# Performance work log

Hardware: AMD Instinct MI355X
Metric: run time of the kernel (lower is better)

## Reference

```python
import jax, jax.numpy as jnp
import numpy as np

TOP_K = 8  # num_experts_per_tok


def setup_inputs() -> dict:
    key = jax.random.key(0)
    k1, k2, k3 = jax.random.split(key, 3)
    B, S, H, E = 4, 4096, 2048, 64
    hidden_states = jax.random.normal(k1, (B, S, H), dtype=jnp.float32)
    router_weight = jax.random.normal(k2, (E, H), dtype=jnp.float32)
    router_bias = jnp.zeros((E,), dtype=jnp.float32)
    expert_bias = jax.random.normal(k3, (E, H), dtype=jnp.float32) * 0.1
    return {
        "hidden_states": hidden_states,
        "router_weight": router_weight,
        "router_bias": router_bias,
        "expert_bias": expert_bias,
    }


def reference(hidden_states, router_weight, router_bias, expert_bias):
    B, S, H = hidden_states.shape
    flat = hidden_states.reshape(B * S, H)  # [T, H]
    # Router: linear -> softmax -> top-k
    logits = jnp.einsum("th,eh->te", flat, router_weight) + router_bias
    scores = jax.nn.softmax(logits, axis=-1)
    topk_w, topk_idx = jax.lax.top_k(scores, TOP_K)  # [T, K]
    # Dispatch/combine collapses to: combined[t,k] = x[t] + expert_bias[idx[t,k]]
    # output[t] = sum_k w[t,k] * combined[t,k]
    #          = x[t] * sum_k w[t,k] + sum_k w[t,k] * expert_bias[idx[t,k]]
    gathered_bias = expert_bias[topk_idx]  # [T, K, H]
    out = flat * jnp.sum(topk_w, axis=-1, keepdims=True) + jnp.einsum(
        "tk,tkh->th", topk_w, gathered_bias
    )
    return out.reshape(B, S, H)
```

## Files before the change

kernel.cpp:

```cpp
#include <hip/hip_runtime.h>
#include <hip/hip_bf16.h>
#include <float.h>

#define H 2048
#define E 64
#define TOPK 8
#define RT 16
#define TT 8
#define NT 512

typedef __attribute__((ext_vector_type(8))) short bf16x8;
typedef __attribute__((ext_vector_type(4))) float f32x4;
typedef __attribute__((ext_vector_type(4))) unsigned short us4;

__device__ __forceinline__ unsigned short f2bf(float f) {
  unsigned u = __float_as_uint(f);
  u += 0x7fffu + ((u >> 16) & 1u);
  return (unsigned short)(u >> 16);
}
__device__ __forceinline__ float bf2f(unsigned short s) {
  return __uint_as_float(((unsigned)s) << 16);
}
__device__ __forceinline__ float wred_max(float v) {
#pragma unroll
  for (int o = 32; o > 0; o >>= 1) v = fmaxf(v, __shfl_xor(v, o));
  return v;
}
__device__ __forceinline__ float wred_sum(float v) {
#pragma unroll
  for (int o = 32; o > 0; o >>= 1) v += __shfl_xor(v, o);
  return v;
}

__global__ __launch_bounds__(256) void cvt_kernel(const float* __restrict__ W,
                                                  const float* __restrict__ eb,
                                                  unsigned short* __restrict__ Wb,
                                                  unsigned short* __restrict__ Bb) {
  int i = (blockIdx.x * 256 + threadIdx.x) * 4;
  const float* src;
  unsigned short* dst;
  int off;
  if (i < E * H) { src = W; dst = Wb; off = i; }
  else           { src = eb; dst = Bb; off = i - E * H; }
  float4 v = *(const float4*)(src + off);
  us4 r;
  r[0] = f2bf(v.x); r[1] = f2bf(v.y); r[2] = f2bf(v.z); r[3] = f2bf(v.w);
  *(us4*)(dst + off) = r;
}

__global__ __launch_bounds__(256, 4) void router_kernel(
    const float* __restrict__ x, const unsigned short* __restrict__ Wb,
    const float* __restrict__ rb, float* __restrict__ msw_g,
    float* __restrict__ mw_g, int* __restrict__ mi_g) {
  __shared__ float lgs[4][RT][E + 1];
  const int tid = threadIdx.x;
  const int wv = tid >> 6, lane = tid & 63, quad = lane >> 4, m = lane & 15;
  const int t0 = (blockIdx.x * 4 + wv) * RT;

  f32x4 acc0 = {0.f,0.f,0.f,0.f}, acc1 = {0.f,0.f,0.f,0.f};
  f32x4 acc2 = {0.f,0.f,0.f,0.f}, acc3 = {0.f,0.f,0.f,0.f};
  const float* xp = x + (size_t)(t0 + m) * H + quad * 8;
  const unsigned short* wp = Wb + (size_t)m * H + quad * 8;
#pragma unroll 4
  for (int it = 0; it < H / 32; ++it) {
    float4 p = *(const float4*)(xp + it * 32);
    float4 q = *(const float4*)(xp + it * 32 + 4);
    bf16x8 av;
    av[0] = (short)f2bf(p.x); av[1] = (short)f2bf(p.y);
    av[2] = (short)f2bf(p.z); av[3] = (short)f2bf(p.w);
    av[4] = (short)f2bf(q.x); av[5] = (short)f2bf(q.y);
    av[6] = (short)f2bf(q.z); av[7] = (short)f2bf(q.w);
    bf16x8 b0 = *(const bf16x8*)(wp + (size_t)0 * 16 * H + it * 32);
    bf16x8 b1 = *(const bf16x8*)(wp + (size_t)1 * 16 * H + it * 32);
    bf16x8 b2 = *(const bf16x8*)(wp + (size_t)2 * 16 * H + it * 32);
    bf16x8 b3 = *(const bf16x8*)(wp + (size_t)3 * 16 * H + it * 32);
    acc0 = __builtin_amdgcn_mfma_f32_16x16x32_bf16(av, b0, acc0, 0, 0, 0);
    acc1 = __builtin_amdgcn_mfma_f32_16x16x32_bf16(av, b1, acc1, 0, 0, 0);
    acc2 = __builtin_amdgcn_mfma_f32_16x16x32_bf16(av, b2, acc2, 0, 0, 0);
    acc3 = __builtin_amdgcn_mfma_f32_16x16x32_bf16(av, b3, acc3, 0, 0, 0);
  }
#pragma unroll
  for (int r = 0; r < 4; ++r) {
    const int row = quad * 4 + r;
    lgs[wv][row][ 0 + m] = acc0[r];
    lgs[wv][row][16 + m] = acc1[r];
    lgs[wv][row][32 + m] = acc2[r];
    lgs[wv][row][48 + m] = acc3[r];
  }
  const float rbl = rb[lane];
  for (int t = 0; t < RT; ++t) {
    float l = lgs[wv][t][lane] + rbl;
    const float mx = wred_max(l);
    const float p = expf(l - mx);
    const float inv = 1.f / wred_sum(p);
    float sumw = 0.f, lsel = l;
    float mywk = 0.f;
    int myoff = 0;
#pragma unroll
    for (int k = 0; k < TOPK; ++k) {
      const float mk = wred_max(lsel);
      const unsigned long long b = __ballot(lsel == mk);
      const int idx = __ffsll(b) - 1;
      const float wk = expf(mk - mx) * inv;
      sumw += wk;
      if (lane == k) { mywk = wk; myoff = idx * H; }
      if (lane == idx) lsel = -FLT_MAX;
    }
    const int tt = t0 + t;
    if (lane == 0) msw_g[tt] = sumw;
    if (lane < TOPK) {
      mw_g[(size_t)tt * TOPK + lane] = mywk;
      mi_g[(size_t)tt * TOPK + lane] = myoff;
    }
  }
}

__global__ __launch_bounds__(256, 4) void combine_kernel(
    const float* __restrict__ x, const unsigned short* __restrict__ Bb,
    const float* __restrict__ msw_g, const float* __restrict__ mw_g,
    const int* __restrict__ mi_g, float* __restrict__ out) {
  const int tid = threadIdx.x;
  const int wv = tid >> 6, lane = tid & 63;
  const int t = blockIdx.x * 4 + wv;
  const float sw = msw_g[t];
  const float4 w0 = *(const float4*)(mw_g + (size_t)t * TOPK);
  const float4 w1 = *(const float4*)(mw_g + (size_t)t * TOPK + 4);
  const int4  e0 = *(const int4*)(mi_g + (size_t)t * TOPK);
  const int4  e1 = *(const int4*)(mi_g + (size_t)t * TOPK + 4);
  const float wks[8] = {w0.x, w0.y, w0.z, w0.w, w1.x, w1.y, w1.z, w1.w};
  const int   ofs[8] = {e0.x, e0.y, e0.z, e0.w, e1.x, e1.y, e1.z, e1.w};
  const float* xr = x + (size_t)t * H;
  float* orow = out + (size_t)t * H;
#pragma unroll
  for (int ch = 0; ch < 4; ++ch) {
    const int c8 = ch * 512 + lane * 8;
    const float4 xa = *(const float4*)(xr + c8);
    const float4 xb = *(const float4*)(xr + c8 + 4);
    float o[8] = {xa.x * sw, xa.y * sw, xa.z * sw, xa.w * sw,
                  xb.x * sw, xb.y * sw, xb.z * sw, xb.w * sw};
#pragma unroll
    for (int k = 0; k < TOPK; ++k) {
      const bf16x8 bv = *(const bf16x8*)(Bb + ofs[k] + c8);
      const float wk = wks[k];
#pragma unroll
      for (int i = 0; i < 8; ++i) o[i] += wk * bf2f((unsigned short)bv[i]);
    }
    *(float4*)(orow + c8)     = make_float4(o[0], o[1], o[2], o[3]);
    *(float4*)(orow + c8 + 4) = make_float4(o[4], o[5], o[6], o[7]);
  }
}

template <bool USE_WS>
__global__ __launch_bounds__(NT, 8) void moe_kernel(
    const float* __restrict__ x, const float* __restrict__ W,
    const float* __restrict__ rb, const float* __restrict__ eb,
    const unsigned short* __restrict__ Wb, const unsigned short* __restrict__ Bb,
    float* __restrict__ out) {
  __shared__ unsigned short xl[TT][H + 8];
  __shared__ float lgp[2][TT][E + 1];
  __shared__ float msw[TT];
  __shared__ float mw[TT][TOPK];
  __shared__ int   mi[TT][TOPK];

  const int tid = threadIdx.x;
  const int t0  = blockIdx.x * TT;
  const int wv = tid >> 6, lane = tid & 63, quad = lane >> 4, m = lane & 15;

  {
    const float* row = x + (size_t)(t0 + wv) * H;
#pragma unroll
    for (int i = 0; i < 8; ++i) {
      const int c = (i * 64 + lane) * 4;
      float4 a = *(const float4*)(row + c);
      us4 ra;
      ra[0] = f2bf(a.x); ra[1] = f2bf(a.y); ra[2] = f2bf(a.z); ra[3] = f2bf(a.w);
      *(us4*)&xl[wv][c] = ra;
    }
  }
  __syncthreads();

  {
    const int eg = wv & 3, kh = wv >> 2;
    const int e = eg * 16 + m;
    const int k0 = kh * (H / 2);
    f32x4 acc = {0.f, 0.f, 0.f, 0.f};
    const unsigned short* xp = &xl[m & 7][k0 + quad * 8];
    if (USE_WS) {
      const unsigned short* wp = Wb + (size_t)e * H + k0 + quad * 8;
#pragma unroll 8
      for (int it = 0; it < H / 64; ++it) {
        bf16x8 av = *(const bf16x8*)(xp + it * 32);
        bf16x8 bv = *(const bf16x8*)(wp + it * 32);
        acc = __builtin_amdgcn_mfma_f32_16x16x32_bf16(av, bv, acc, 0, 0, 0);
      }
    } else {
      const float* wp = W + (size_t)e * H + k0 + quad * 8;
#pragma unroll 4
      for (int it = 0; it < H / 64; ++it) {
        bf16x8 av = *(const bf16x8*)(xp + it * 32);
        float4 p = *(const float4*)(wp + it * 32);
        float4 q = *(const float4*)(wp + it * 32 + 4);
        bf16x8 bv;
        bv[0] = (short)f2bf(p.x); bv[1] = (short)f2bf(p.y);
        bv[2] = (short)f2bf(p.z); bv[3] = (short)f2bf(p.w);
        bv[4] = (short)f2bf(q.x); bv[5] = (short)f2bf(q.y);
        bv[6] = (short)f2bf(q.z); bv[7] = (short)f2bf(q.w);
        acc = __builtin_amdgcn_mfma_f32_16x16x32_bf16(av, bv, acc, 0, 0, 0);
      }
    }
#pragma unroll
    for (int r = 0; r < 4; ++r) {
      const int row = quad * 4 + r;
      if (row < TT) lgp[kh][row][eg * 16 + m] = acc[r];
    }
  }
  __syncthreads();

  {
    const int t = wv;
    float l = lgp[0][t][lane] + lgp[1][t][lane] + rb[lane];
    const float mx = wred_max(l);
    const float p = expf(l - mx);
    const float inv = 1.f / wred_sum(p);
    float sumw = 0.f;
    float lsel = l;
#pragma unroll
    for (int k = 0; k < TOPK; ++k) {
      const float mk = wred_max(lsel);
      const unsigned long long b = __ballot(lsel == mk);
      const int idx = __ffsll(b) - 1;
      const float wk = expf(mk - mx) * inv;
      sumw += wk;
      if (lane == 0) { mw[t][k] = wk; mi[t][k] = idx * H; }
      if (lane == idx) lsel = -FLT_MAX;
    }
    if (lane == 0) msw[t] = sumw;
  }
  __syncthreads();

  {
    const int tg = tid >> 8;
    const int c8 = (tid & 255) * 8;
    const unsigned short* bbase = Bb + c8;
    const float* ebase = eb + c8;
#pragma unroll 1
    for (int tt = 0; tt < TT / 2; ++tt) {
      const int t = tg * (TT / 2) + tt;
      const float sw = msw[t];
      const float4 w0 = *(const float4*)&mw[t][0];
      const float4 w1 = *(const float4*)&mw[t][4];
      const int4  e0 = *(const int4*)&mi[t][0];
      const int4  e1 = *(const int4*)&mi[t][4];
      const float wks[8] = {w0.x, w0.y, w0.z, w0.w, w1.x, w1.y, w1.z, w1.w};
      const int   ofs[8] = {e0.x, e0.y, e0.z, e0.w, e1.x, e1.y, e1.z, e1.w};
      bf16x8 xv = *(const bf16x8*)&xl[t][c8];
      float o[8];
#pragma unroll
      for (int i = 0; i < 8; ++i) o[i] = bf2f((unsigned short)xv[i]) * sw;
#pragma unroll
      for (int k = 0; k < TOPK; ++k) {
        const float wk = wks[k];
        if (USE_WS) {
          bf16x8 bv = *(const bf16x8*)(bbase + ofs[k]);
#pragma unroll
          for (int i = 0; i < 8; ++i) o[i] += wk * bf2f((unsigned short)bv[i]);
        } else {
          const float* p = ebase + ofs[k];
          float4 p0 = *(const float4*)p;
          float4 p1 = *(const float4*)(p + 4);
          o[0] += wk * p0.x; o[1] += wk * p0.y; o[2] += wk * p0.z; o[3] += wk * p0.w;
          o[4] += wk * p1.x; o[5] += wk * p1.y; o[6] += wk * p1.z; o[7] += wk * p1.w;
        }
      }
      float* op = out + (size_t)(t0 + t) * H + c8;
      *(float4*)op       = make_float4(o[0], o[1], o[2], o[3]);
      *(float4*)(op + 4) = make_float4(o[4], o[5], o[6], o[7]);
    }
  }
}

extern "C" void kernel_launch(void* const* d_in, const int* in_sizes, int n_in,
                              void* d_out, int out_size, void* d_ws, size_t ws_size,
                              hipStream_t stream) {
  const float* x  = (const float*)d_in[0];
  const float* W  = (const float*)d_in[1];
  const float* rb = (const float*)d_in[2];
  const float* eb = (const float*)d_in[3];
  float* out = (float*)d_out;

  const int T = in_sizes[0] / H;
  const size_t szW = (size_t)E * H * sizeof(unsigned short);
  const size_t need_old = 2 * szW;
  const size_t meta_sz = (size_t)T * 4 + (size_t)T * TOPK * 4 * 2;
  const size_t need_new = 2 * szW + meta_sz;

  if (ws_size >= need_new) {
    unsigned short* Wb = (unsigned short*)d_ws;
    unsigned short* Bb = Wb + (size_t)E * H;
    float* msw_g = (float*)(Bb + (size_t)E * H);
    float* mw_g  = msw_g + T;
    int*   mi_g  = (int*)(mw_g + (size_t)T * TOPK);
    cvt_kernel<<<(2 * E * H) / (256 * 4), 256, 0, stream>>>(W, eb, Wb, Bb);
    router_kernel<<<T / (4 * RT), 256, 0, stream>>>(x, Wb, rb, msw_g, mw_g, mi_g);
    combine_kernel<<<T / 4, 256, 0, stream>>>(x, Bb, msw_g, mw_g, mi_g, out);
  } else if (ws_size >= need_old) {
    unsigned short* Wb = (unsigned short*)d_ws;
    unsigned short* Bb = Wb + (size_t)E * H;
    cvt_kernel<<<(2 * E * H) / (256 * 4), 256, 0, stream>>>(W, eb, Wb, Bb);
    moe_kernel<true><<<T / TT, NT, 0, stream>>>(x, W, rb, eb, Wb, Bb, out);
  } else {
    moe_kernel<false><<<T / TT, NT, 0, stream>>>(x, W, rb, eb, nullptr, nullptr, out);
  }
}
```

Measured before the change: 330.7 us.

## Split router K-dimension across eight waves with LDS reduction

The router kernel now gives each 512-thread block 16 tokens and splits the H=2048 reduction across 8 waves. Each wave computes partial logits over a 256-wide K slice, and the partials are summed through shared memory after a barrier. Each wave then runs softmax/top-k for 2 tokens. This raises the grid from 256 to 1024 blocks to improve occupancy and latency hiding on the router GEMV. The cost is an extra block barrier, LDS traffic, and eight-way redundant reads of the weight rows per block.

```diff
diff --git a/kernel.cpp b/kernel.cpp
--- a/kernel.cpp
+++ b/kernel.cpp
@@ -5,7 +5,7 @@
 #define H 2048
 #define E 64
 #define TOPK 8
-#define RT 16
+#define RTOK 16
 #define TT 8
 #define NT 512
 
@@ -48,21 +48,22 @@
   *(us4*)(dst + off) = r;
 }
 
-__global__ __launch_bounds__(256, 4) void router_kernel(
+__global__ __launch_bounds__(512, 4) void router_kernel(
     const float* __restrict__ x, const unsigned short* __restrict__ Wb,
     const float* __restrict__ rb, float* __restrict__ msw_g,
     float* __restrict__ mw_g, int* __restrict__ mi_g) {
-  __shared__ float lgs[4][RT][E + 1];
+  __shared__ float lgs[8][RTOK][E + 1];
   const int tid = threadIdx.x;
   const int wv = tid >> 6, lane = tid & 63, quad = lane >> 4, m = lane & 15;
-  const int t0 = (blockIdx.x * 4 + wv) * RT;
+  const int t0 = blockIdx.x * RTOK;
+  const int k0 = wv * (H / 8);
 
   f32x4 acc0 = {0.f,0.f,0.f,0.f}, acc1 = {0.f,0.f,0.f,0.f};
   f32x4 acc2 = {0.f,0.f,0.f,0.f}, acc3 = {0.f,0.f,0.f,0.f};
-  const float* xp = x + (size_t)(t0 + m) * H + quad * 8;
-  const unsigned short* wp = Wb + (size_t)m * H + quad * 8;
-#pragma unroll 4
-  for (int it = 0; it < H / 32; ++it) {
+  const float* xp = x + (size_t)(t0 + m) * H + k0 + quad * 8;
+  const unsigned short* wp = Wb + (size_t)m * H + k0 + quad * 8;
+#pragma unroll
+  for (int it = 0; it < H / 8 / 32; ++it) {
     float4 p = *(const float4*)(xp + it * 32);
     float4 q = *(const float4*)(xp + it * 32 + 4);
     bf16x8 av;
@@ -87,9 +88,15 @@
     lgs[wv][row][32 + m] = acc2[r];
     lgs[wv][row][48 + m] = acc3[r];
   }
+  __syncthreads();
+
   const float rbl = rb[lane];
-  for (int t = 0; t < RT; ++t) {
-    float l = lgs[wv][t][lane] + rbl;
+#pragma unroll
+  for (int tt = 0; tt < 2; ++tt) {
+    const int t = wv * 2 + tt;
+    float l = rbl;
+#pragma unroll
+    for (int kq = 0; kq < 8; ++kq) l += lgs[kq][t][lane];
     const float mx = wred_max(l);
     const float p = expf(l - mx);
     const float inv = 1.f / wred_sum(p);
@@ -106,11 +113,11 @@
       if (lane == k) { mywk = wk; myoff = idx * H; }
       if (lane == idx) lsel = -FLT_MAX;
     }
-    const int tt = t0 + t;
-    if (lane == 0) msw_g[tt] = sumw;
+    const int tg = t0 + t;
+    if (lane == 0) msw_g[tg] = sumw;
     if (lane < TOPK) {
-      mw_g[(size_t)tt * TOPK + lane] = mywk;
-      mi_g[(size_t)tt * TOPK + lane] = myoff;
+      mw_g[(size_t)tg * TOPK + lane] = mywk;
+      mi_g[(size_t)tg * TOPK + lane] = myoff;
     }
   }
 }
@@ -301,7 +308,7 @@
     float* mw_g  = msw_g + T;
     int*   mi_g  = (int*)(mw_g + (size_t)T * TOPK);
     cvt_kernel<<<(2 * E * H) / (256 * 4), 256, 0, stream>>>(W, eb, Wb, Bb);
-    router_kernel<<<T / (4 * RT), 256, 0, stream>>>(x, Wb, rb, msw_g, mw_g, mi_g);
+    router_kernel<<<T / RTOK, 512, 0, stream>>>(x, Wb, rb, msw_g, mw_g, mi_g);
     combine_kernel<<<T / 4, 256, 0, stream>>>(x, Bb, msw_g, mw_g, mi_g, out);
   } else if (ws_size >= need_old) {
     unsigned short* Wb = (unsigned short*)d_ws;
```

Measured after the change: 280.9 us. 1.18x faster.
